# Kernel optimization log

Hardware: AMD Instinct MI355X
Metric: run time of the kernel (lower is better)

Reference implementation:

```python
import jax, jax.numpy as jnp
from jax import lax
import numpy as np

B = 32768
H = 7
W = 7
EMB = 64
NUM_ACTIONS = 7
HIDDEN = 128
CNN_OUT = 64 * 3 * 3  # 576, from 7x7 input through the conv/pool stack


def setup_inputs() -> dict:
    key = jax.random.key(0)
    ks = jax.random.split(key, 20)
    frame = jax.random.randint(ks[0], (2, B, H, W, 3), 0, 11, dtype=jnp.int32)
    carried_col = jax.random.randint(ks[1], (2, B, 1), 0, 6, dtype=jnp.int32)
    carried_obj = jax.random.randint(ks[2], (2, B, 1), 0, 11, dtype=jnp.int32)

    def w(k, shape):
        return (jax.random.normal(k, shape, jnp.float32) * 0.05)

    return {
        "frame": frame,
        "carried_col": carried_col,
        "carried_obj": carried_obj,
        "conv1_w": w(ks[3], (16, 3, 2, 2)),  "conv1_b": jnp.zeros((16,), jnp.float32),
        "conv2_w": w(ks[4], (32, 16, 2, 2)), "conv2_b": jnp.zeros((32,), jnp.float32),
        "conv3_w": w(ks[5], (64, 32, 2, 2)), "conv3_b": jnp.zeros((64,), jnp.float32),
        "proj_w": w(ks[6], (EMB, CNN_OUT + 2)), "proj_b": jnp.zeros((EMB,), jnp.float32),
        "h1_w": w(ks[7], (HIDDEN, EMB * 2 + 4)), "h1_b": jnp.zeros((HIDDEN,), jnp.float32),
        "ln_g": jnp.ones((HIDDEN,), jnp.float32), "ln_b": jnp.zeros((HIDDEN,), jnp.float32),
        "h2_w": w(ks[8], (HIDDEN, HIDDEN)), "h2_b": jnp.zeros((HIDDEN,), jnp.float32),
        "h3_w": w(ks[9], (NUM_ACTIONS, HIDDEN)), "h3_b": jnp.zeros((NUM_ACTIONS,), jnp.float32),
    }


def _conv(x, wgt, b):
    # Conv2d(kernel=2, padding=1), NCHW
    y = lax.conv_general_dilated(x, wgt, (1, 1), [(1, 1), (1, 1)],
                                 dimension_numbers=("NCHW", "OIHW", "NCHW"))
    return y + b[None, :, None, None]


def _maxpool2(x):
    # MaxPool2d(2): window 2, stride 2, floor (VALID)
    return lax.reduce_window(x, -jnp.inf, lax.max, (1, 1, 2, 2), (1, 1, 2, 2), "VALID")


def _encode(fr, cc, co, p):
    x = fr.transpose(0, 3, 1, 2).astype(jnp.float32)  # [B,3,H,W]
    x = _maxpool2(jax.nn.relu(_conv(x, p["conv1_w"], p["conv1_b"])))  # [B,16,4,4]
    x = _maxpool2(jax.nn.relu(_conv(x, p["conv2_w"], p["conv2_b"])))  # [B,32,2,2]
    x = jax.nn.relu(_conv(x, p["conv3_w"], p["conv3_b"]))             # [B,64,3,3]
    feats = x.reshape(x.shape[0], -1)                                  # [B,576]
    carried = jnp.concatenate([cc, co], axis=-1).astype(jnp.float32)   # [B,2]
    comb = jnp.concatenate([feats, carried], axis=1)                   # [B,578]
    return jax.nn.relu(comb @ p["proj_w"].T + p["proj_b"])            # [B,64]


def _dir_pos(fr):
    # vectorized first-match of frame[...,0]==10 in row-major order
    b = fr.shape[0]
    mask = (fr[..., 0] == 10).reshape(b, -1)             # [B, H*W]
    has = jnp.any(mask, axis=-1)                         # [B]
    idx = jnp.argmax(mask, axis=-1)                      # first True (row-major)
    y = idx // W
    x = idx % W
    ch2 = fr[..., 2].reshape(b, -1)
    d_raw = jnp.take_along_axis(ch2, idx[:, None], axis=1)[:, 0] % 4
    d = jnp.where(has, d_raw, 0)                         # [B] int
    pos = jnp.stack([y.astype(jnp.float32) / (H - 1),
                     x.astype(jnp.float32) / (W - 1)], axis=-1)
    pos = jnp.where(has[:, None], pos, jnp.float32(0.5))  # [B,2]
    return d, pos


def _forward(frame, carried_col, carried_obj, p):
    curr_f, next_f = frame[0], frame[1]
    curr_emb = _encode(curr_f, carried_col[0], carried_obj[0], p)
    next_emb = _encode(next_f, carried_col[1], carried_obj[1], p)
    cd, cpos = _dir_pos(curr_f)
    nd, npos = _dir_pos(next_f)
    delta = ((nd - cd + 4) % 4).astype(jnp.float32)
    angle = delta * (2.0 * 3.14159 / 4.0)  # matches source constant
    dir_delta = jnp.stack([jnp.sin(angle), jnp.cos(angle)], axis=-1)  # [B,2]
    pos_delta = npos - cpos                                           # [B,2]
    comb = jnp.concatenate([curr_emb, next_emb, dir_delta, pos_delta], axis=-1)  # [B,132]
    h = comb @ p["h1_w"].T + p["h1_b"]
    mu = h.mean(-1, keepdims=True)
    var = ((h - mu) ** 2).mean(-1, keepdims=True)
    h = (h - mu) * lax.rsqrt(var + 1e-5) * p["ln_g"] + p["ln_b"]
    h = jax.nn.relu(h)  # dropout = identity in eval
    h = jax.nn.relu(h @ p["h2_w"].T + p["h2_b"])
    return h @ p["h3_w"].T + p["h3_b"]  # [B, num_actions]


def reference(frame, carried_col, carried_obj,
              conv1_w, conv1_b, conv2_w, conv2_b, conv3_w, conv3_b,
              proj_w, proj_b, h1_w, h1_b, ln_g, ln_b,
              h2_w, h2_b, h3_w, h3_b):
    p = dict(conv1_w=conv1_w, conv1_b=conv1_b, conv2_w=conv2_w, conv2_b=conv2_b,
             conv3_w=conv3_w, conv3_b=conv3_b, proj_w=proj_w, proj_b=proj_b,
             h1_w=h1_w, h1_b=h1_b, ln_g=ln_g, ln_b=ln_b,
             h2_w=h2_w, h2_b=h2_b, h3_w=h3_w, h3_b=h3_b)
    return _forward(frame, carried_col, carried_obj, p)
```

## Files before the change

### kernel.cpp

```cpp
#include <hip/hip_runtime.h>
#include <hip/hip_bf16.h>

#define BATCH 32768
#define NELEM 65536

typedef unsigned short u16;
typedef unsigned int u32;
typedef __attribute__((ext_vector_type(8))) short bf16x8;
typedef __attribute__((ext_vector_type(4))) float f32x4;

__device__ __forceinline__ float bf2f(u16 u) {
    union { u32 u; float f; } c; c.u = ((u32)u) << 16; return c.f;
}
__device__ __forceinline__ u16 f2bf(float f) {
    union { float f; u32 u; } c; c.f = f;
    u32 x = c.u;
    u32 r = (x + 0x7fffu + ((x >> 16) & 1u)) >> 16;
    return (u16)r;
}

__global__ __launch_bounds__(256) void k0_prep(const float* __restrict__ pw,
        const float* __restrict__ w2, const float* __restrict__ w3,
        const float* __restrict__ h2w, const float* __restrict__ h1w,
        const float* __restrict__ w1,
        u16* __restrict__ pwT, u16* __restrict__ w2r, u16* __restrict__ w3r,
        u16* __restrict__ h2hi, u16* __restrict__ h2lo,
        u16* __restrict__ h1hi, u16* __restrict__ h1lo,
        u16* __restrict__ w1hi, u16* __restrict__ w1lo) {
    int idx = blockIdx.x * 256 + threadIdx.x;
    if (idx < 38912) {
        int j = idx / 608, kk = idx - j * 608;
        float v = 0.f;
        if (kk < 576) {
            int p = kk >> 6, oc = kk & 63;
            v = pw[j * 578 + oc * 9 + p];
        } else if (kk < 578) {
            v = pw[j * 578 + kk];
        }
        pwT[idx] = f2bf(v);
    } else if (idx < 40960) {
        int i = idx - 38912;
        int oc = i >> 6, rem = i & 63, tap = rem >> 4, ic = rem & 15;
        w2r[i] = f2bf(w2[oc * 64 + ic * 4 + tap]);
    } else if (idx < 49152) {
        int i = idx - 40960;
        int oc = i >> 7, rem = i & 127, tap = rem >> 5, ic = rem & 31;
        w3r[i] = f2bf(w3[oc * 128 + ic * 4 + tap]);
    } else if (idx < 65536) {
        int i = idx - 49152;
        float v = h2w[i];
        u16 hi = f2bf(v);
        h2hi[i] = hi;
        h2lo[i] = f2bf(v - bf2f(hi));
    } else if (idx < 86016) {
        int i = idx - 65536;
        int j = i / 160, k = i - j * 160;
        float v = (k < 132) ? h1w[j * 132 + k] : 0.f;
        u16 hi = f2bf(v);
        h1hi[i] = hi;
        h1lo[i] = f2bf(v - bf2f(hi));
    } else if (idx < 86528) {
        int i = idx - 86016;
        int oc = i >> 5, k = i & 31;
        int ky = k >> 4, kx = (k >> 3) & 1, c = k & 7;
        float v = (c < 3) ? w1[oc * 12 + c * 4 + ky * 2 + kx] : 0.f;
        u16 hi = f2bf(v);
        w1hi[i] = hi;
        w1lo[i] = f2bf(v - bf2f(hi));
    }
}

__global__ __launch_bounds__(256) void kconv_all(const int* __restrict__ frame,
        const u16* __restrict__ w1hi, const u16* __restrict__ w1lo,
        const float* __restrict__ b1,
        const u16* __restrict__ w2r, const float* __restrict__ b2,
        const u16* __restrict__ w3r, const float* __restrict__ b3,
        const int* __restrict__ ccol, const int* __restrict__ cobj,
        const u16* __restrict__ pwT, const float* __restrict__ pb,
        float* __restrict__ comb) {
    __shared__ u16 lds[24576];
    u16* p2L   = lds;
    u16* p1L   = lds + 4096;
    u16* frL   = lds + 12288;
    u16* featL = lds + 4096;
    int t = threadIdx.x;
    int l = t & 63;
    int wv = t >> 6;
    int col = l & 15;
    int kg = l >> 4;
    int e0 = blockIdx.x * 32;

    #pragma unroll
    for (int i = 0; i < 6; ++i) {
        int o = i * 256 + t;
        if (o < 1312) *(uint4*)(frL + o * 8) = make_uint4(0u, 0u, 0u, 0u);
    }

    {
        bf16x8 c1hi = *(const bf16x8*)(w1hi + col * 32 + kg * 8);
        bf16x8 c1lo = *(const bf16x8*)(w1lo + col * 32 + kg * 8);
        float c1b = b1[col];
        int ky1 = kg >> 1, kx1 = kg & 1;
        bool wr1 = (kg < 2);
        for (int h = 0; h < 2; ++h) {
            __syncthreads();
            const int* fbase = frame + (size_t)(e0 + h * 16) * 147;
            #pragma unroll
            for (int i = 0; i < 10; ++i) {
                int idx = i * 256 + t;
                if (idx < 2352) {
                    int le = idx / 147, r = idx - le * 147;
                    int cell = r / 3, c = r - cell * 3;
                    int y = cell / 7, x = cell - y * 7;
                    frL[le * 656 + (y + 1) * 72 + (x + 1) * 8 + c] = f2bf((float)fbase[idx]);
                }
            }
            __syncthreads();
            #pragma unroll
            for (int q = 0; q < 4; ++q) {
                int le = wv * 4 + q;
                const u16* eb = frL + le * 656;
                u16* op = p1L + (h * 16 + le) * 256;
                #pragma unroll
                for (int mt = 0; mt < 4; ++mt) {
                    int posA = mt * 16 + col;
                    int oy = posA >> 3, ox = posA & 7;
                    bf16x8 a = *(const bf16x8*)(eb + (oy + ky1) * 72 + (ox + kx1) * 8);
                    f32x4 acc = {0.f, 0.f, 0.f, 0.f};
                    acc = __builtin_amdgcn_mfma_f32_16x16x32_bf16(a, c1hi, acc, 0, 0, 0);
                    acc = __builtin_amdgcn_mfma_f32_16x16x32_bf16(a, c1lo, acc, 0, 0, 0);
                    float x0 = fmaxf(acc[0] + c1b, 0.f);
                    float x1 = fmaxf(acc[1] + c1b, 0.f);
                    float x2 = fmaxf(acc[2] + c1b, 0.f);
                    float x3 = fmaxf(acc[3] + c1b, 0.f);
                    float y0 = fmaxf(x0, x1);
                    float y1 = fmaxf(x2, x3);
                    float m0 = fmaxf(y0, __shfl_xor(y0, 32, 64));
                    float m1 = fmaxf(y1, __shfl_xor(y1, 32, 64));
                    if (wr1) {
                        op[(mt * 4 + kg * 2 + 0) * 16 + col] = f2bf(m0);
                        op[(mt * 4 + kg * 2 + 1) * 16 + col] = f2bf(m1);
                    }
                }
            }
        }
    }
    __syncthreads();

    {
        bf16x8 bfrag[2][2];
        #pragma unroll
        for (int s = 0; s < 2; ++s)
            #pragma unroll
            for (int nt = 0; nt < 2; ++nt)
                bfrag[s][nt] = *(const bf16x8*)(w2r + (nt * 16 + col) * 64 + s * 32 + kg * 8);
        float bias2[2] = { b2[col], b2[16 + col] };
        int oy = col >> 2, ox = col & 3;
        int aoff[2]; bool aok[2];
        #pragma unroll
        for (int s = 0; s < 2; ++s) {
            int tap = 2 * s + (kg >> 1);
            int ky = tap >> 1, kx = tap & 1;
            int iy = oy - 1 + ky, ix = ox - 1 + kx;
            aok[s] = (iy >= 0 && ix >= 0);
            aoff[s] = (iy * 4 + ix) * 16 + (kg & 1) * 8;
        }
        #pragma unroll
        for (int q = 0; q < 8; ++q) {
            int e = wv * 8 + q;
            const u16* pbase = p1L + e * 256;
            bf16x8 a0 = {0,0,0,0,0,0,0,0}, a1 = {0,0,0,0,0,0,0,0};
            if (aok[0]) a0 = *(const bf16x8*)(pbase + aoff[0]);
            if (aok[1]) a1 = *(const bf16x8*)(pbase + aoff[1]);
            f32x4 acc0 = {0.f,0.f,0.f,0.f}, acc1 = {0.f,0.f,0.f,0.f};
            acc0 = __builtin_amdgcn_mfma_f32_16x16x32_bf16(a0, bfrag[0][0], acc0, 0, 0, 0);
            acc1 = __builtin_amdgcn_mfma_f32_16x16x32_bf16(a0, bfrag[0][1], acc1, 0, 0, 0);
            acc0 = __builtin_amdgcn_mfma_f32_16x16x32_bf16(a1, bfrag[1][0], acc0, 0, 0, 0);
            acc1 = __builtin_amdgcn_mfma_f32_16x16x32_bf16(a1, bfrag[1][1], acc1, 0, 0, 0);
            #pragma unroll
            for (int nt = 0; nt < 2; ++nt) {
                f32x4 acc = nt ? acc1 : acc0;
                float b = bias2[nt];
                float m0 = fmaxf(fmaxf(acc[0] + b, 0.f), fmaxf(acc[1] + b, 0.f));
                float m1 = fmaxf(fmaxf(acc[2] + b, 0.f), fmaxf(acc[3] + b, 0.f));
                float p0 = fmaxf(m0, __shfl_xor(m0, 16, 64));
                float p1 = fmaxf(m1, __shfl_xor(m1, 16, 64));
                if ((kg & 1) == 0) {
                    int qq = (kg >> 1) * 2;
                    u16* op = p2L + e * 128 + nt * 16 + col;
                    op[qq * 32]       = f2bf(p0);
                    op[(qq + 1) * 32] = f2bf(p1);
                }
            }
        }
    }
    __syncthreads();

    int colhi = col >> 3, collo = col & 7;
    {
        bf16x8 bfrag[4][4];
        #pragma unroll
        for (int s = 0; s < 4; ++s)
            #pragma unroll
            for (int nt = 0; nt < 4; ++nt)
                bfrag[s][nt] = *(const bf16x8*)(w3r + (nt * 16 + col) * 128 + s * 32 + kg * 8);
        float bias[4];
        #pragma unroll
        for (int nt = 0; nt < 4; ++nt) bias[nt] = b3[nt * 16 + col];

        auto do_tile = [&](int i) {
            int m0 = i * 16;
            int m = m0 + col;
            u32 elem = (u32)(((unsigned long long)(u32)m * 954437177ull) >> 33);
            int p = m - (int)elem * 9;
            int oy = (p * 86) >> 8;
            int ox = p - 3 * oy;
            const u16* pbase = p2L + elem * 128 + kg * 8;
            f32x4 acc[4];
            #pragma unroll
            for (int nt = 0; nt < 4; ++nt) {
                acc[nt][0] = 0.f; acc[nt][1] = 0.f; acc[nt][2] = 0.f; acc[nt][3] = 0.f;
            }
            #pragma unroll
            for (int s = 0; s < 4; ++s) {
                int ky = s >> 1, kx = s & 1;
                int iy = oy - 1 + ky, ix = ox - 1 + kx;
                bf16x8 a = {0,0,0,0,0,0,0,0};
                if (iy >= 0 && iy <= 1 && ix >= 0 && ix <= 1)
                    a = *(const bf16x8*)(pbase + (iy * 2 + ix) * 32);
                #pragma unroll
                for (int nt = 0; nt < 4; ++nt)
                    acc[nt] = __builtin_amdgcn_mfma_f32_16x16x32_bf16(a, bfrag[s][nt], acc[nt], 0, 0, 0);
            }
            #pragma unroll
            for (int r = 0; r < 4; ++r) {
                int mr = m0 + kg * 4 + r;
                u32 er = (u32)(((unsigned long long)(u32)mr * 954437177ull) >> 33);
                int pr = mr - (int)er * 9;
                int e7 = (int)(er & 7u);
                u16* fb = featL + er * 640 + collo;
                #pragma unroll
                for (int nt = 0; nt < 4; ++nt) {
                    int blk = (pr * 8 + nt * 2 + colhi) ^ e7;
                    fb[blk * 8] = f2bf(fmaxf(acc[nt][r] + bias[nt], 0.f));
                }
            }
        };
        #pragma unroll
        for (int u = 0; u < 4; ++u) do_tile(wv + u * 4);
        if (wv < 2) do_tile(16 + wv);
    }
    if (t < 32) {
        union { u16 s[8]; uint4 q; } b;
        b.s[0] = f2bf((float)ccol[e0 + t]);
        b.s[1] = f2bf((float)cobj[e0 + t]);
        #pragma unroll
        for (int i = 2; i < 8; ++i) b.s[i] = 0;
        *(uint4*)(featL + t * 640 + (72 ^ (t & 7)) * 8) = b.q;
    }
    __syncthreads();

    int rh = wv & 1, nh = wv >> 1;
    int m0g = e0 + rh * 16;
    const u16* arowb = featL + (rh * 16 + col) * 640;
    int rx = col & 7;
    const u16* brow = pwT + (nh * 32 + col) * 608 + kg * 8;
    f32x4 acc0 = {0.f,0.f,0.f,0.f}, acc1 = {0.f,0.f,0.f,0.f};
    #pragma unroll
    for (int k0 = 0; k0 < 608; k0 += 32) {
        bf16x8 a;
        if (k0 + kg * 8 < 584) {
            int L = (k0 >> 3) + kg;
            a = *(const bf16x8*)(arowb + (L ^ rx) * 8);
        } else {
            #pragma unroll
            for (int j = 0; j < 8; ++j) a[j] = 0;
        }
        bf16x8 b0 = *(const bf16x8*)(brow + k0);
        bf16x8 b1 = *(const bf16x8*)(brow + 16 * 608 + k0);
        acc0 = __builtin_amdgcn_mfma_f32_16x16x32_bf16(a, b0, acc0, 0, 0, 0);
        acc1 = __builtin_amdgcn_mfma_f32_16x16x32_bf16(a, b1, acc1, 0, 0, 0);
    }
    float* outbase = (m0g < BATCH) ? (comb + (size_t)m0g * 160)
                                   : (comb + (size_t)(m0g - BATCH) * 160 + 64);
    #pragma unroll
    for (int nt = 0; nt < 2; ++nt) {
        int n = nh * 32 + nt * 16 + col;
        float pbv = pb[n];
        f32x4 acc = nt ? acc1 : acc0;
        #pragma unroll
        for (int r = 0; r < 4; ++r) {
            outbase[(kg * 4 + r) * 160 + n] = fmaxf(acc[r] + pbv, 0.f);
        }
    }
}

__global__ __launch_bounds__(256) void k5_extras(const int* __restrict__ frame,
        float* __restrict__ comb) {
    int b = blockIdx.x * 256 + threadIdx.x;
    int d[2]; float posy[2], posx[2];
    for (int f = 0; f < 2; ++f) {
        const int* fb = frame + (size_t)(f * BATCH + b) * 147;
        int idx = 49;
        for (int cell = 0; cell < 49; ++cell) {
            int v = fb[cell * 3];
            if (idx == 49 && v == 10) idx = cell;
        }
        if (idx < 49) {
            d[f] = fb[idx * 3 + 2] & 3;
            posy[f] = (float)(idx / 7) / 6.0f;
            posx[f] = (float)(idx % 7) / 6.0f;
        } else {
            d[f] = 0; posy[f] = 0.5f; posx[f] = 0.5f;
        }
    }
    int delta = (d[1] - d[0] + 4) & 3;
    const float ANG = (float)(2.0 * 3.14159 / 4.0);
    float angle = (float)delta * ANG;
    float4 o;
    o.x = sinf(angle);
    o.y = cosf(angle);
    o.z = posy[1] - posy[0];
    o.w = posx[1] - posx[0];
    float* cb = comb + (size_t)b * 160 + 128;
    *(float4*)cb = o;
    float4 z = make_float4(0.f, 0.f, 0.f, 0.f);
    #pragma unroll
    for (int i = 1; i < 8; ++i) *(float4*)(cb + i * 4) = z;
}

__device__ __forceinline__ void split8(const float* __restrict__ x,
                                       bf16x8& hi, bf16x8& lo) {
    #pragma unroll
    for (int j = 0; j < 8; ++j) {
        u16 h = f2bf(x[j]);
        hi[j] = (short)h;
        lo[j] = (short)f2bf(x[j] - bf2f(h));
    }
}

__global__ __launch_bounds__(256) void kmlp(const float* __restrict__ comb,
        const u16* __restrict__ h1hi, const u16* __restrict__ h1lo,
        const float* __restrict__ h1b,
        const float* __restrict__ lng, const float* __restrict__ lnb,
        const u16* __restrict__ h2hi, const u16* __restrict__ h2lo,
        const float* __restrict__ h2b,
        const float* __restrict__ h3w, const float* __restrict__ h3b,
        float* __restrict__ out) {
    __shared__ float hL[64 * 132];
    int t = threadIdx.x;
    int l = t & 63;
    int col = l & 15;
    int kg = l >> 4;
    int wv = t >> 6;
    int mb = blockIdx.x * 64;

    {
        const float* arow = comb + (size_t)(mb + wv * 16 + col) * 160 + kg * 8;
        const u16* bh = h1hi + col * 160 + kg * 8;
        const u16* bl = h1lo + col * 160 + kg * 8;
        f32x4 acc[8];
        #pragma unroll
        for (int nt = 0; nt < 8; ++nt) {
            acc[nt][0] = 0.f; acc[nt][1] = 0.f; acc[nt][2] = 0.f; acc[nt][3] = 0.f;
        }
        #pragma unroll
        for (int s = 0; s < 5; ++s) {
            float x[8];
            #pragma unroll
            for (int j = 0; j < 8; ++j) x[j] = arow[s * 32 + j];
            bf16x8 ahi, alo;
            split8(x, ahi, alo);
            #pragma unroll
            for (int nt = 0; nt < 8; ++nt) {
                bf16x8 bhiF = *(const bf16x8*)(bh + nt * 2560 + s * 32);
                bf16x8 bloF = *(const bf16x8*)(bl + nt * 2560 + s * 32);
                acc[nt] = __builtin_amdgcn_mfma_f32_16x16x32_bf16(ahi, bhiF, acc[nt], 0, 0, 0);
                acc[nt] = __builtin_amdgcn_mfma_f32_16x16x32_bf16(alo, bhiF, acc[nt], 0, 0, 0);
                acc[nt] = __builtin_amdgcn_mfma_f32_16x16x32_bf16(ahi, bloF, acc[nt], 0, 0, 0);
            }
        }
        #pragma unroll
        for (int nt = 0; nt < 8; ++nt) {
            float bv = h1b[nt * 16 + col];
            #pragma unroll
            for (int r = 0; r < 4; ++r)
                hL[(wv * 16 + kg * 4 + r) * 132 + nt * 16 + col] = acc[nt][r] + bv;
        }
    }
    __syncthreads();

    for (int rr = 0; rr < 16; ++rr) {
        float* rp = hL + (wv * 16 + rr) * 132 + l * 2;
        float2 v = *(const float2*)rp;
        float s = v.x + v.y;
        s += __shfl_xor(s, 1, 64);
        s += __shfl_xor(s, 2, 64);
        s += __shfl_xor(s, 4, 64);
        s += __shfl_xor(s, 8, 64);
        s += __shfl_xor(s, 16, 64);
        s += __shfl_xor(s, 32, 64);
        float mu = s * (1.0f / 128.0f);
        float d0 = v.x - mu, d1 = v.y - mu;
        float vs = d0 * d0 + d1 * d1;
        vs += __shfl_xor(vs, 1, 64);
        vs += __shfl_xor(vs, 2, 64);
        vs += __shfl_xor(vs, 4, 64);
        vs += __shfl_xor(vs, 8, 64);
        vs += __shfl_xor(vs, 16, 64);
        vs += __shfl_xor(vs, 32, 64);
        float rs = rsqrtf(vs * (1.0f / 128.0f) + 1e-5f);
        float2 o;
        o.x = fmaxf(d0 * rs * lng[l * 2]     + lnb[l * 2],     0.f);
        o.y = fmaxf(d1 * rs * lng[l * 2 + 1] + lnb[l * 2 + 1], 0.f);
        *(float2*)rp = o;
    }
    __syncthreads();

    {
        const float* arow = hL + (wv * 16 + col) * 132 + kg * 8;
        const u16* bh = h2hi + col * 128 + kg * 8;
        const u16* bl = h2lo + col * 128 + kg * 8;
        f32x4 acc[8];
        #pragma unroll
        for (int nt = 0; nt < 8; ++nt) {
            acc[nt][0] = 0.f; acc[nt][1] = 0.f; acc[nt][2] = 0.f; acc[nt][3] = 0.f;
        }
        #pragma unroll
        for (int s = 0; s < 4; ++s) {
            float x[8];
            #pragma unroll
            for (int j = 0; j < 8; ++j) x[j] = arow[s * 32 + j];
            bf16x8 ahi, alo;
            split8(x, ahi, alo);
            #pragma unroll
            for (int nt = 0; nt < 8; ++nt) {
                bf16x8 bhiF = *(const bf16x8*)(bh + nt * 2048 + s * 32);
                bf16x8 bloF = *(const bf16x8*)(bl + nt * 2048 + s * 32);
                acc[nt] = __builtin_amdgcn_mfma_f32_16x16x32_bf16(ahi, bhiF, acc[nt], 0, 0, 0);
                acc[nt] = __builtin_amdgcn_mfma_f32_16x16x32_bf16(alo, bhiF, acc[nt], 0, 0, 0);
                acc[nt] = __builtin_amdgcn_mfma_f32_16x16x32_bf16(ahi, bloF, acc[nt], 0, 0, 0);
            }
        }
        #pragma unroll
        for (int nt = 0; nt < 8; ++nt) {
            float bv = h2b[nt * 16 + col];
            #pragma unroll
            for (int r = 0; r < 4; ++r)
                hL[(wv * 16 + kg * 4 + r) * 132 + nt * 16 + col] = fmaxf(acc[nt][r] + bv, 0.f);
        }
    }
    __syncthreads();

    {
        int row = t >> 2, jq = t & 3, j0 = jq * 2;
        const float* rp = hL + row * 132;
        float a0 = h3b[j0];
        float a1 = (jq < 3) ? h3b[j0 + 1] : 0.f;
        #pragma unroll 4
        for (int c = 0; c < 32; ++c) {
            float4 v = *(const float4*)(rp + c * 4);
            const float* wr0 = h3w + j0 * 128 + c * 4;
            a0 += v.x * wr0[0];
            a0 += v.y * wr0[1];
            a0 += v.z * wr0[2];
            a0 += v.w * wr0[3];
            if (jq < 3) {
                const float* wr1 = h3w + (j0 + 1) * 128 + c * 4;
                a1 += v.x * wr1[0];
                a1 += v.y * wr1[1];
                a1 += v.z * wr1[2];
                a1 += v.w * wr1[3];
            }
        }
        float* ob = out + (size_t)(mb + row) * 7;
        ob[j0] = a0;
        if (jq < 3) ob[j0 + 1] = a1;
    }
}

extern "C" void kernel_launch(void* const* d_in, const int* in_sizes, int n_in,
                              void* d_out, int out_size, void* d_ws, size_t ws_size,
                              hipStream_t stream) {
    const int*   frame = (const int*)d_in[0];
    const int*   ccol  = (const int*)d_in[1];
    const int*   cobj  = (const int*)d_in[2];
    const float* w1    = (const float*)d_in[3];
    const float* b1    = (const float*)d_in[4];
    const float* w2    = (const float*)d_in[5];
    const float* b2    = (const float*)d_in[6];
    const float* w3    = (const float*)d_in[7];
    const float* b3    = (const float*)d_in[8];
    const float* pw    = (const float*)d_in[9];
    const float* pb    = (const float*)d_in[10];
    const float* h1w   = (const float*)d_in[11];
    const float* h1b   = (const float*)d_in[12];
    const float* lng   = (const float*)d_in[13];
    const float* lnb   = (const float*)d_in[14];
    const float* h2w   = (const float*)d_in[15];
    const float* h2b   = (const float*)d_in[16];
    const float* h3w   = (const float*)d_in[17];
    const float* h3b   = (const float*)d_in[18];
    float* out = (float*)d_out;

    char* ws = (char*)d_ws;
    float* comb     = (float*)(ws + 0);
    u16*   pwT      = (u16*)(ws + 132120576);
    u16*   w2r      = (u16*)(ws + 132120576 + 131072);
    u16*   w3r      = (u16*)(ws + 132120576 + 139264);
    u16*   h2hi     = (u16*)(ws + 132120576 + 163840);
    u16*   h2lo     = (u16*)(ws + 132120576 + 196608);
    u16*   h1hi     = (u16*)(ws + 132120576 + 229376);
    u16*   h1lo     = (u16*)(ws + 132120576 + 270336);
    u16*   w1hi     = (u16*)(ws + 132120576 + 311296);
    u16*   w1lo     = (u16*)(ws + 132120576 + 312320);

    k0_prep<<<340, 256, 0, stream>>>(pw, w2, w3, h2w, h1w, w1,
                                     pwT, w2r, w3r, h2hi, h2lo, h1hi, h1lo,
                                     w1hi, w1lo);
    kconv_all<<<2048, 256, 0, stream>>>(frame, w1hi, w1lo, b1, w2r, b2,
                                        w3r, b3, ccol, cobj, pwT, pb, comb);
    k5_extras<<<128, 256, 0, stream>>>(frame, comb);
    kmlp<<<512, 256, 0, stream>>>(comb, h1hi, h1lo, h1b, lng, lnb,
                                  h2hi, h2lo, h2b, h3w, h3b, out);
}
```

Measured before the change: 248.8 us.

## Fuse agent direction/position extraction into conv kernel and shrink comb rows

Removes the separate k5_extras kernel, which re-read the full int32 frame with a serial per-thread scan. The agent-cell search now runs inside the conv kernel on the frame tile already staged in LDS, using a wave shuffle min-reduction, and writes a small float4 per frame to a side buffer. The MLP kernel computes the sin/cos direction delta and position delta itself, so comb rows shrink from 160 to 128 floats, cutting global traffic. It adds work and a __syncthreads to kmlp and extra LDS reads in conv.

Measured after the change: 231.0 us. 7.2% less time.

```diff
diff --git a/kernel.cpp b/kernel.cpp
--- a/kernel.cpp
+++ b/kernel.cpp
@@ -77,7 +77,7 @@
         const u16* __restrict__ w3r, const float* __restrict__ b3,
         const int* __restrict__ ccol, const int* __restrict__ cobj,
         const u16* __restrict__ pwT, const float* __restrict__ pb,
-        float* __restrict__ comb) {
+        float* __restrict__ comb, float4* __restrict__ fdir) {
     __shared__ u16 lds[24576];
     u16* p2L   = lds;
     u16* p1L   = lds + 4096;
@@ -143,6 +143,35 @@
                     }
                 }
             }
+            {
+                int le = wv * 4 + kg;
+                const u16* eb = frL + le * 656;
+                int best = 49;
+                #pragma unroll
+                for (int q2 = 0; q2 < 4; ++q2) {
+                    int cell = col + q2 * 16;
+                    if (cell < 49) {
+                        int y = cell / 7, x = cell - y * 7;
+                        u16 v = eb[(y + 1) * 72 + (x + 1) * 8];
+                        if (v == (u16)0x4120 && cell < best) best = cell;
+                    }
+                }
+                best = min(best, __shfl_xor(best, 1, 64));
+                best = min(best, __shfl_xor(best, 2, 64));
+                best = min(best, __shfl_xor(best, 4, 64));
+                best = min(best, __shfl_xor(best, 8, 64));
+                if (col == 0) {
+                    float dd = 0.f, py = 0.5f, px = 0.5f;
+                    if (best < 49) {
+                        int y = best / 7, x = best - y * 7;
+                        u16 c2 = eb[(y + 1) * 72 + (x + 1) * 8 + 2];
+                        dd = (float)(((int)bf2f(c2)) & 3);
+                        py = (float)y / 6.0f;
+                        px = (float)x / 6.0f;
+                    }
+                    fdir[e0 + h * 16 + le] = make_float4(dd, py, px, 0.f);
+                }
+            }
         }
     }
     __syncthreads();
@@ -281,8 +310,8 @@
         acc0 = __builtin_amdgcn_mfma_f32_16x16x32_bf16(a, b0, acc0, 0, 0, 0);
         acc1 = __builtin_amdgcn_mfma_f32_16x16x32_bf16(a, b1, acc1, 0, 0, 0);
     }
-    float* outbase = (m0g < BATCH) ? (comb + (size_t)m0g * 160)
-                                   : (comb + (size_t)(m0g - BATCH) * 160 + 64);
+    float* outbase = (m0g < BATCH) ? (comb + (size_t)m0g * 128)
+                                   : (comb + (size_t)(m0g - BATCH) * 128 + 64);
     #pragma unroll
     for (int nt = 0; nt < 2; ++nt) {
         int n = nh * 32 + nt * 16 + col;
@@ -290,43 +319,9 @@
         f32x4 acc = nt ? acc1 : acc0;
         #pragma unroll
         for (int r = 0; r < 4; ++r) {
-            outbase[(kg * 4 + r) * 160 + n] = fmaxf(acc[r] + pbv, 0.f);
-        }
-    }
-}
-
-__global__ __launch_bounds__(256) void k5_extras(const int* __restrict__ frame,
-        float* __restrict__ comb) {
-    int b = blockIdx.x * 256 + threadIdx.x;
-    int d[2]; float posy[2], posx[2];
-    for (int f = 0; f < 2; ++f) {
-        const int* fb = frame + (size_t)(f * BATCH + b) * 147;
-        int idx = 49;
-        for (int cell = 0; cell < 49; ++cell) {
-            int v = fb[cell * 3];
-            if (idx == 49 && v == 10) idx = cell;
-        }
-        if (idx < 49) {
-            d[f] = fb[idx * 3 + 2] & 3;
-            posy[f] = (float)(idx / 7) / 6.0f;
-            posx[f] = (float)(idx % 7) / 6.0f;
-        } else {
-            d[f] = 0; posy[f] = 0.5f; posx[f] = 0.5f;
-        }
-    }
-    int delta = (d[1] - d[0] + 4) & 3;
-    const float ANG = (float)(2.0 * 3.14159 / 4.0);
-    float angle = (float)delta * ANG;
-    float4 o;
-    o.x = sinf(angle);
-    o.y = cosf(angle);
-    o.z = posy[1] - posy[0];
-    o.w = posx[1] - posx[0];
-    float* cb = comb + (size_t)b * 160 + 128;
-    *(float4*)cb = o;
-    float4 z = make_float4(0.f, 0.f, 0.f, 0.f);
-    #pragma unroll
-    for (int i = 1; i < 8; ++i) *(float4*)(cb + i * 4) = z;
+            outbase[(kg * 4 + r) * 128 + n] = fmaxf(acc[r] + pbv, 0.f);
+        }
+    }
 }
 
 __device__ __forceinline__ void split8(const float* __restrict__ x,
@@ -340,6 +335,7 @@
 }
 
 __global__ __launch_bounds__(256) void kmlp(const float* __restrict__ comb,
+        const float4* __restrict__ fdir,
         const u16* __restrict__ h1hi, const u16* __restrict__ h1lo,
         const float* __restrict__ h1b,
         const float* __restrict__ lng, const float* __restrict__ lnb,
@@ -356,7 +352,8 @@
     int mb = blockIdx.x * 64;
 
     {
-        const float* arow = comb + (size_t)(mb + wv * 16 + col) * 160 + kg * 8;
+        int gb = mb + wv * 16 + col;
+        const float* arow = comb + (size_t)gb * 128 + kg * 8;
         const u16* bh = h1hi + col * 160 + kg * 8;
         const u16* bl = h1lo + col * 160 + kg * 8;
         f32x4 acc[8];
@@ -367,8 +364,24 @@
         #pragma unroll
         for (int s = 0; s < 5; ++s) {
             float x[8];
-            #pragma unroll
-            for (int j = 0; j < 8; ++j) x[j] = arow[s * 32 + j];
+            if (s < 4) {
+                #pragma unroll
+                for (int j = 0; j < 8; ++j) x[j] = arow[s * 32 + j];
+            } else {
+                #pragma unroll
+                for (int j = 0; j < 8; ++j) x[j] = 0.f;
+                if (kg == 0) {
+                    float4 f0 = fdir[gb];
+                    float4 f1 = fdir[gb + BATCH];
+                    int delta = (((int)f1.x) - ((int)f0.x) + 4) & 3;
+                    const float ANG = (float)(2.0 * 3.14159 / 4.0);
+                    float angle = (float)delta * ANG;
+                    x[0] = sinf(angle);
+                    x[1] = cosf(angle);
+                    x[2] = f1.y - f0.y;
+                    x[3] = f1.z - f0.z;
+                }
+            }
             bf16x8 ahi, alo;
             split8(x, ahi, alo);
             #pragma unroll
@@ -442,6 +455,7 @@
                 acc[nt] = __builtin_amdgcn_mfma_f32_16x16x32_bf16(ahi, bloF, acc[nt], 0, 0, 0);
             }
         }
+        __syncthreads();
         #pragma unroll
         for (int nt = 0; nt < 8; ++nt) {
             float bv = h2b[nt * 16 + col];
@@ -505,6 +519,7 @@
 
     char* ws = (char*)d_ws;
     float* comb     = (float*)(ws + 0);
+    float4* fdir    = (float4*)(ws + 33554432);
     u16*   pwT      = (u16*)(ws + 132120576);
     u16*   w2r      = (u16*)(ws + 132120576 + 131072);
     u16*   w3r      = (u16*)(ws + 132120576 + 139264);
@@ -519,8 +534,7 @@
                                      pwT, w2r, w3r, h2hi, h2lo, h1hi, h1lo,
                                      w1hi, w1lo);
     kconv_all<<<2048, 256, 0, stream>>>(frame, w1hi, w1lo, b1, w2r, b2,
-                                        w3r, b3, ccol, cobj, pwT, pb, comb);
-    k5_extras<<<128, 256, 0, stream>>>(frame, comb);
-    kmlp<<<512, 256, 0, stream>>>(comb, h1hi, h1lo, h1b, lng, lnb,
+                                        w3r, b3, ccol, cobj, pwT, pb, comb, fdir);
+    kmlp<<<512, 256, 0, stream>>>(comb, fdir, h1hi, h1lo, h1b, lng, lnb,
                                   h2hi, h2lo, h2b, h3w, h3b, out);
 }
```
